# Kernel optimization log

Measured on AMD Instinct MI355X. Metric: run time of the kernel, lower is better.

The kernel has to match this reference:

```python
import jax, jax.numpy as jnp
import numpy as np
import math

# Static config (mirrors init_kwargs)
E, B, S, D, F, HMAX = 8, 4, 1024, 1024, 4096, 8
W = 768                      # active slimmable width (multiple giving integer head_dim)
H = max(1, W * HMAX // D)    # = 6 heads at width 768
HD = W // H                  # = 128
TOPK = 2
EPS = 1e-6


def setup_inputs() -> dict:
    key = jax.random.key(0)
    ks = jax.random.split(key, 14)
    sd = 1.0 / math.sqrt(D)
    sf = 1.0 / math.sqrt(F)
    return {
        "x":  jax.random.normal(ks[0], (B, S, D), jnp.float32),
        "wr": jax.random.normal(ks[1], (D, E), jnp.float32) * sd,
        "qw": jax.random.normal(ks[2], (E, D, D), jnp.float32) * sd,
        "qb": jax.random.normal(ks[3], (E, D), jnp.float32) * sd,
        "kw": jax.random.normal(ks[4], (E, D, D), jnp.float32) * sd,
        "kb": jax.random.normal(ks[5], (E, D), jnp.float32) * sd,
        "vw": jax.random.normal(ks[6], (E, D, D), jnp.float32) * sd,
        "vb": jax.random.normal(ks[7], (E, D), jnp.float32) * sd,
        "ow": jax.random.normal(ks[8], (E, D, D), jnp.float32) * sd,
        "ob": jax.random.normal(ks[9], (E, D), jnp.float32) * sd,
        "w1": jax.random.normal(ks[10], (E, F, D), jnp.float32) * sd,
        "b1": jax.random.normal(ks[11], (E, F), jnp.float32) * sd,
        "w2": jax.random.normal(ks[12], (E, D, F), jnp.float32) * sf,
        "b2": jax.random.normal(ks[13], (E, D), jnp.float32) * sf,
    }


def _slim_linear(x, w, b, in_w, out_w):
    # SlimmableLinear: dynamically slice max-size weight/bias to active widths
    return x @ w[:out_w, :in_w].T + b[:out_w]


def _rms_norm(x):
    # SlimmableExpert._layer_norm: RMS normalization (no mean-subtract, no affine)
    var = jnp.mean(jnp.square(x), axis=-1, keepdims=True)
    return x / jnp.sqrt(var + EPS)


def _expert_fwd(x_s, qw, qb, kw, kb, vw, vb, ow, ob, w1, b1, w2, b2):
    # x_s: [B, S, W]  (already sliced to active width)
    # --- slimmable self-attention at width W ---
    q = _slim_linear(x_s, qw, qb, W, W).reshape(B, S, H, HD).transpose(0, 2, 1, 3)
    k = _slim_linear(x_s, kw, kb, W, W).reshape(B, S, H, HD).transpose(0, 2, 1, 3)
    v = _slim_linear(x_s, vw, vb, W, W).reshape(B, S, H, HD).transpose(0, 2, 1, 3)
    scores = jnp.einsum('bhqd,bhkd->bhqk', q, k) / math.sqrt(HD)   # [B,H,S,S]
    attn = jax.nn.softmax(scores, axis=-1)
    ao = jnp.einsum('bhqk,bhkd->bhqd', attn, v)
    ao = ao.transpose(0, 2, 1, 3).reshape(B, S, W)
    ao = _slim_linear(ao, ow, ob, W, W)
    x1 = _rms_norm(x_s + ao)
    # --- slimmable FFN: W -> F (full) -> W, exact GELU (torch default) ---
    h = jax.nn.gelu(_slim_linear(x1, w1, b1, W, F), approximate=False)
    f = _slim_linear(h, w2, b2, F, W)
    return _rms_norm(x1 + f)   # [B,S,W]


def reference(x, wr, qw, qb, kw, kb, vw, vb, ow, ob, w1, b1, w2, b2):
    # Router: softmax over experts, top-k dispatch with renormalized gates
    logits = jnp.einsum('bsd,de->bse', x, wr)            # [B,S,E]
    probs = jax.nn.softmax(logits, axis=-1)
    topv, topi = jax.lax.top_k(probs, TOPK)              # [B,S,K]
    topv = topv / jnp.sum(topv, axis=-1, keepdims=True)
    bi = jnp.arange(B)[:, None, None]
    si = jnp.arange(S)[None, :, None]
    gate = jnp.zeros((B, S, E), x.dtype).at[bi, si, topi].set(topv)  # sparse gate

    # Slice tokens to active width (width embedding skipped: closest stored
    # width 736 != 768, per source shape-match check)
    x_s = x[..., :W]
    outs = []
    for e in range(E):   # small fixed expert count; bounds peak memory
        outs.append(_expert_fwd(x_s, qw[e], qb[e], kw[e], kb[e], vw[e], vb[e],
                                ow[e], ob[e], w1[e], b1[e], w2[e], b2[e]))
    eo = jnp.stack(outs, axis=0)                          # [E,B,S,W]
    out_w = jnp.einsum('bse,ebsw->bsw', gate, eo)         # gate-weighted combine
    # Zero-pad sliced width back to full model dim (per SlimmableExpert)
    out = jnp.concatenate(
        [out_w, jnp.zeros((B, S, D - W), x.dtype)], axis=-1)
    return out
```

## Files before the change

### kernel.cpp

```cpp
#include <hip/hip_runtime.h>
#include <cstdint>

#define NE 8
#define NB 4
#define NS 1024
#define ND 1024
#define NF 4096
#define NW 768
#define NH 6
#define NHD 128
#define NTOK 4096
#define NBH 24
#define RCAP 10496
#define VSTRIDE ((size_t)NTOK * NW)
#define EPS 1e-6f

typedef unsigned short ush;
typedef __attribute__((ext_vector_type(8))) short short8;
typedef __attribute__((ext_vector_type(4))) float f32x4;
typedef __attribute__((ext_vector_type(4))) unsigned short u16x4;

typedef const __attribute__((address_space(1))) void gvoid_t;
typedef __attribute__((address_space(3))) void lvoid_t;

__device__ __forceinline__ void gload16(const void* g, void* l) {
  __builtin_amdgcn_global_load_lds((gvoid_t*)g, (lvoid_t*)l, 16, 0, 0);
}

__device__ __forceinline__ ush f2b(float f) {
  union { float f; uint32_t u; } x; x.f = f;
  uint32_t r = x.u + 0x7fffu + ((x.u >> 16) & 1u);
  return (ush)(r >> 16);
}
__device__ __forceinline__ float b2f(ush u) {
  union { uint32_t u; float f; } x; x.u = (uint32_t)u << 16;
  return x.f;
}
__device__ __forceinline__ int prefix_sum(const int* __restrict__ c, int n) {
  int s = 0;
#pragma unroll 1
  for (int i = 0; i < n; ++i) s += c[i];
  return s;
}

__global__ __launch_bounds__(256, 4)
void router_kernel(const float* __restrict__ x, const float* __restrict__ wr,
                   float* __restrict__ gate, int* __restrict__ inv) {
  int lane = threadIdx.x & 63, wave = threadIdx.x >> 6;
  int t = blockIdx.x * 4 + wave;
  float acc[NE] = {};
  for (int i = 0; i < 16; ++i) {
    int d = lane + i * 64;
    float xv = x[(size_t)t * ND + d];
    const float* wp = wr + (size_t)d * NE;
    float4 w0 = *(const float4*)wp, w1 = *(const float4*)(wp + 4);
    acc[0] += xv * w0.x; acc[1] += xv * w0.y; acc[2] += xv * w0.z; acc[3] += xv * w0.w;
    acc[4] += xv * w1.x; acc[5] += xv * w1.y; acc[6] += xv * w1.z; acc[7] += xv * w1.w;
  }
#pragma unroll
  for (int e = 0; e < NE; ++e)
    for (int m = 1; m < 64; m <<= 1) acc[e] += __shfl_xor(acc[e], m);
  int i1 = 0; float v1 = acc[0];
#pragma unroll
  for (int e = 1; e < NE; ++e) if (acc[e] > v1) { v1 = acc[e]; i1 = e; }
  int i2 = -1; float v2 = -3.0e38f;
#pragma unroll
  for (int e = 0; e < NE; ++e) if (e != i1 && acc[e] > v2) { v2 = acc[e]; i2 = e; }
  float p2 = __expf(v2 - v1);
  float g1 = 1.0f / (1.0f + p2), g2 = p2 / (1.0f + p2);
  if (lane < NE)
    gate[(size_t)t * NE + lane] = (lane == i1) ? g1 : ((lane == i2) ? g2 : 0.0f);
  if (lane < 2) inv[t * 2 + lane] = -1;
}

__global__ __launch_bounds__(1024, 1)
void build_index(const float* __restrict__ gate, int* __restrict__ cnt64s,
                 int* __restrict__ idx_all, int* __restrict__ inv) {
  int e = blockIdx.x >> 2, b = blockIdx.x & 3;
  int s = threadIdx.x, t = b * 1024 + s;
  bool on = gate[(size_t)t * NE + e] > 0.0f;
  idx_all[(e * 4 + b) * 1024 + s] = (b * 1024) | (int)0x80000000;
  __shared__ int wsum[16], wbase[16];
  unsigned long long mask = __ballot(on);
  int lane = s & 63, wv = s >> 6;
  if (lane == 0) wsum[wv] = __popcll(mask);
  __syncthreads();
  if (s == 0) {
    int acc = 0;
    for (int i = 0; i < 16; ++i) { wbase[i] = acc; acc += wsum[i]; }
    cnt64s[e * 4 + b] = (acc + 63) & ~63;
  }
  __syncthreads();
  if (on) {
    int pos = wbase[wv] + __popcll(mask & ((1ull << lane) - 1ull));
    idx_all[(e * 4 + b) * 1024 + pos] = t;
    int k = 0;
#pragma unroll
    for (int j = 0; j < NE; ++j) k += (j < e && gate[(size_t)t * NE + j] > 0.0f);
    inv[t * 2 + k] = (e << 12) | pos;
  }
}

__global__ __launch_bounds__(256, 4)
void cast_all(const float* __restrict__ x,
              const float* __restrict__ qw, const float* __restrict__ kw,
              const float* __restrict__ vw, const float* __restrict__ ow,
              const float* __restrict__ w1, const float* __restrict__ w2,
              ush* __restrict__ xs,
              ush* __restrict__ dq, ush* __restrict__ dk, ush* __restrict__ dv,
              ush* __restrict__ dwo, ush* __restrict__ d1, ush* __restrict__ d2) {
  int y = blockIdx.y;
  if (y == 8) {
    const int n4 = NTOK * NW / 4;
    for (int u = blockIdx.x * 256 + threadIdx.x; u < n4; u += gridDim.x * 256) {
      int r = u / (NW / 4), c = u - r * (NW / 4);
      float4 v = *(const float4*)(x + (size_t)r * ND + c * 4);
      u16x4 o; o.x = f2b(v.x); o.y = f2b(v.y); o.z = f2b(v.z); o.w = f2b(v.w);
      *(u16x4*)(xs + (size_t)u * 4) = o;
    }
    return;
  }
  const int e = y;
  const int Q4 = 147456;
  const int W14 = 786432;
  const int total = 4 * Q4 + 2 * W14;
  const float* qe = qw + (size_t)e * ND * ND;
  const float* ke = kw + (size_t)e * ND * ND;
  const float* ve = vw + (size_t)e * ND * ND;
  const float* oe = ow + (size_t)e * ND * ND;
  const float* w1e = w1 + (size_t)e * NF * ND;
  const float* w2e = w2 + (size_t)e * ND * NF;
  ush* dqe = dq + (size_t)e * NW * NW;
  ush* dke = dk + (size_t)e * NW * NW;
  ush* dve = dv + (size_t)e * NW * NW;
  ush* doe = dwo + (size_t)e * NW * NW;
  ush* d1e = d1 + (size_t)e * NF * NW;
  ush* d2e = d2 + (size_t)e * NW * NF;
  for (int u = blockIdx.x * 256 + threadIdx.x; u < total; u += gridDim.x * 256) {
    const float* src; ush* dst; int ldsrc, cols4, rel;
    if (u < 4 * Q4) {
      int which = u / Q4; rel = u - which * Q4;
      src = (which == 0) ? qe : (which == 1) ? ke : (which == 2) ? ve : oe;
      dst = (which == 0) ? dqe : (which == 1) ? dke : (which == 2) ? dve : doe;
      ldsrc = 1024; cols4 = 192;
    } else if (u < 4 * Q4 + W14) {
      rel = u - 4 * Q4; src = w1e; dst = d1e; ldsrc = 1024; cols4 = 192;
    } else {
      rel = u - 4 * Q4 - W14; src = w2e; dst = d2e; ldsrc = 4096; cols4 = 1024;
    }
    int r = rel / cols4, c = rel - r * cols4;
    float4 v = *(const float4*)(src + (size_t)r * ldsrc + (size_t)c * 4);
    u16x4 o; o.x = f2b(v.x); o.y = f2b(v.y); o.z = f2b(v.z); o.w = f2b(v.w);
    *(u16x4*)(dst + (size_t)rel * 4) = o;
  }
}

#define BM 128
#define BN 128
#define BK 64

__device__ __forceinline__ float gelu_exact(float v) {
  return 0.5f * v * (1.0f + erff(v * 0.70710678118654752f));
}

__global__ __launch_bounds__(256, 3)
void qkv_gemm(const ush* __restrict__ A,
              const ush* __restrict__ wqb, const ush* __restrict__ wkb,
              const ush* __restrict__ wvb,
              const float* __restrict__ qbias, const float* __restrict__ kbias,
              const float* __restrict__ vbias,
              ush* __restrict__ qg, ush* __restrict__ kg, ush* __restrict__ vtg,
              const int* __restrict__ cnt64s, const int* __restrict__ idx_all) {
  const int bid = blockIdx.x;
  const int e = bid & 7, wi = bid >> 3;
  const int bn = wi % 6, bm = (wi / 6) % 32, w = wi / 192;
  int sb = 0, cnt = 0;
  if (w == 0) {
    int sec = e * 4 + (bm >> 3);
    cnt = cnt64s[sec];
    if (((bm & 7) * 128) >= cnt) return;
    sb = prefix_sum(cnt64s, sec);
  }
  const ush* Bw = ((w == 0) ? wqb : (w == 1) ? wkb : wvb) + (size_t)e * NW * NW;
  const float* bias = ((w == 0) ? qbias : (w == 1) ? kbias : vbias) + (size_t)e * ND;

  __shared__ __align__(16) ush As[BM * BK];
  __shared__ __align__(16) ush Bs[BN * BK];

  const int tid = threadIdx.x, lane = tid & 63, wave = tid >> 6;
  const int lr = lane & 15, lg = lane >> 4;
  const int wr = wave >> 1, wc = wave & 1;

  int rowIdx[4];
#pragma unroll
  for (int p = 0; p < 4; ++p) {
    if (w == 0) {
      int lrow = (bm & 7) * 128 + p * 32 + (tid >> 3);
      rowIdx[p] = idx_all[(e * 4 + (bm >> 3)) * 1024 + lrow] & 0x7fffffff;
    } else {
      rowIdx[p] = bm * BM + p * 32 + (tid >> 3);
    }
  }

  f32x4 acc[4][4] = {};
  for (int kt = 0; kt < NW / BK; ++kt) {
    __syncthreads();
#pragma unroll
    for (int p = 0; p < 4; ++p) {
      int o = p * 4096 + tid * 16;
      int row = o >> 7, cb = o & 127;
      int cbs = cb ^ ((row & 7) << 4);
      gload16((const char*)A + ((size_t)rowIdx[p] * NW + (size_t)kt * BK) * 2 + cbs,
              (char*)As + o);
      gload16((const char*)Bw + ((size_t)(bn * BN + row) * NW + (size_t)kt * BK) * 2 + cbs,
              (char*)Bs + o);
    }
    __syncthreads();
#pragma unroll
    for (int kk = 0; kk < 2; ++kk) {
      short8 af[4], bfr[4];
#pragma unroll
      for (int i = 0; i < 4; ++i) {
        int rowa = wr * 64 + i * 16 + lr;
        af[i] = *(const short8*)((const char*)As + rowa * 128 +
                                 (((kk * 64 + lg * 16)) ^ ((rowa & 7) << 4)));
        int rowb = wc * 64 + i * 16 + lr;
        bfr[i] = *(const short8*)((const char*)Bs + rowb * 128 +
                                  (((kk * 64 + lg * 16)) ^ ((rowb & 7) << 4)));
      }
#pragma unroll
      for (int i = 0; i < 4; ++i)
#pragma unroll
        for (int j = 0; j < 4; ++j)
          acc[i][j] = __builtin_amdgcn_mfma_f32_16x16x32_bf16(af[i], bfr[j], acc[i][j], 0, 0, 0);
    }
  }

#pragma unroll
  for (int i = 0; i < 4; ++i) {
    int lm16 = (bm & 7) * 128 + wr * 64 + i * 16;
    int m0 = bm * BM + wr * 64 + i * 16 + lg * 4;
#pragma unroll
    for (int j = 0; j < 4; ++j) {
      int n = bn * BN + wc * 64 + j * 16 + lr;
      float bb = bias[n];
      if (w == 0) {
        if (lm16 < cnt) {
          int grow = sb + lm16 + lg * 4;
#pragma unroll
          for (int r = 0; r < 4; ++r)
            qg[(size_t)(grow + r) * NW + n] = f2b(acc[i][j][r] + bb);
        }
      } else if (w == 1) {
        ush* o = kg + (size_t)e * NTOK * NW;
#pragma unroll
        for (int r = 0; r < 4; ++r)
          o[(size_t)(m0 + r) * NW + n] = f2b(acc[i][j][r] + bb);
      } else {
        int b_ = m0 >> 10, s0 = m0 & 1023, h_ = n >> 7, d = n & 127;
        u16x4 wv_;
#pragma unroll
        for (int r = 0; r < 4; ++r) wv_[r] = f2b(acc[i][j][r] + bb);
        *(u16x4*)(vtg + (size_t)e * VSTRIDE +
                  ((size_t)(b_ * NH + h_) * NHD + d) * NS + s0) = wv_;
      }
    }
  }
}

__global__ __launch_bounds__(256, 3)
void attn2(const ush* __restrict__ Qg, const ush* __restrict__ Kg,
           const ush* __restrict__ VTg,
           ush* __restrict__ po, float* __restrict__ mlm, float* __restrict__ mll,
           const int* __restrict__ cnt64s) {
  const int bid = blockIdx.x;
  const int e = bid & 7, wi = bid >> 3;
  const int qb = wi & 15, yy = wi >> 4;
  const int bh = yy >> 2, half = yy & 3;
  const int b = bh / NH, h = bh % NH;
  const int sec = e * 4 + b;
  const int cnt = cnt64s[sec];
  if (qb * 64 >= cnt) return;
  const int sb = prefix_sum(cnt64s, sec);

  __shared__ __align__(16) ush Ks[64 * 128];
  __shared__ __align__(16) ush VTs[128 * 64];
  __shared__ __align__(16) ush Ps[4 * 16 * 64];

  const int tid = threadIdx.x, lane = tid & 63, wave = tid >> 6;
  const int lr = lane & 15, lg = lane >> 4;
  const int k0 = half * 256;
  const float cexp = 1.4426950408889634f / sqrtf((float)NHD);

  const ush* Ke = Kg + (size_t)e * NTOK * NW;
  const ush* Ve = VTg + (size_t)e * VSTRIDE;

  int growq = sb + qb * 64 + wave * 16 + lr;
  short8 qf[4];
#pragma unroll
  for (int kk = 0; kk < 4; ++kk)
    qf[kk] = *(const short8*)(Qg + (size_t)growq * NW + h * NHD + kk * 32 + lg * 8);

  f32x4 accv[8] = {};
  float mr[4] = {-3.0e38f, -3.0e38f, -3.0e38f, -3.0e38f};
  float ls[4] = {};

  for (int kt = 0; kt < 4; ++kt) {
    __syncthreads();
#pragma unroll
    for (int p = 0; p < 4; ++p) {
      int o = p * 4096 + tid * 16;
      int row = o >> 8, cb = o & 255;
      gload16((const char*)Ke + ((size_t)(b * NS + k0 + kt * 64 + row) * NW + h * NHD) * 2 +
                  (cb ^ ((row & 7) << 4)),
              (char*)Ks + o);
    }
#pragma unroll
    for (int p = 0; p < 4; ++p) {
      int o = p * 4096 + tid * 16;
      int d = o >> 7, cb = o & 127;
      gload16((const char*)Ve + ((size_t)((b * NH + h) * NHD + d) * NS + k0 + kt * 64) * 2 +
                  (cb ^ ((d & 7) << 4)),
              (char*)VTs + o);
    }
    __syncthreads();

    f32x4 s[4] = {};
#pragma unroll
    for (int kg2 = 0; kg2 < 4; ++kg2)
#pragma unroll
      for (int kk = 0; kk < 4; ++kk) {
        int row = kg2 * 16 + lr;
        short8 kf = *(const short8*)((const char*)Ks + row * 256 +
                                     ((kk * 64 + lg * 16) ^ ((row & 7) << 4)));
        s[kg2] = __builtin_amdgcn_mfma_f32_16x16x32_bf16(qf[kk], kf, s[kg2], 0, 0, 0);
      }

    float mt[4];
#pragma unroll
    for (int r = 0; r < 4; ++r) {
      float m0 = fmaxf(fmaxf(s[0][r], s[1][r]), fmaxf(s[2][r], s[3][r]));
#pragma unroll
      for (int mm = 1; mm < 16; mm <<= 1) m0 = fmaxf(m0, __shfl_xor(m0, mm));
      mt[r] = m0;
    }
    bool need = (mt[0] > mr[0] + 8.f) || (mt[1] > mr[1] + 8.f) ||
                (mt[2] > mr[2] + 8.f) || (mt[3] > mr[3] + 8.f);
    if (__any(need)) {
#pragma unroll
      for (int r = 0; r < 4; ++r) {
        float mn = fmaxf(mr[r], mt[r]);
        float sc = exp2f((mr[r] - mn) * cexp);
        mr[r] = mn; ls[r] *= sc;
#pragma unroll
        for (int dg = 0; dg < 8; ++dg) accv[dg][r] *= sc;
      }
    }

    char* pw = (char*)Ps + wave * 2048;
#pragma unroll
    for (int kg2 = 0; kg2 < 4; ++kg2)
#pragma unroll
      for (int r = 0; r < 4; ++r) {
        float p = exp2f((s[kg2][r] - mr[r]) * cexp);
        ls[r] += p;
        int row = lg * 4 + r;
        *(ush*)(pw + row * 128 + (((kg2 * 16 + lr) * 2) ^ ((row & 7) << 4))) = f2b(p);
      }
    short8 pf[2];
#pragma unroll
    for (int kk2 = 0; kk2 < 2; ++kk2)
      pf[kk2] = *(const short8*)(pw + lr * 128 + ((kk2 * 64 + lg * 16) ^ ((lr & 7) << 4)));

#pragma unroll
    for (int dg = 0; dg < 8; ++dg) {
      int d = dg * 16 + lr;
#pragma unroll
      for (int kk2 = 0; kk2 < 2; ++kk2) {
        short8 vf = *(const short8*)((const char*)VTs + d * 128 +
                                     ((kk2 * 64 + lg * 16) ^ ((d & 7) << 4)));
        accv[dg] = __builtin_amdgcn_mfma_f32_16x16x32_bf16(pf[kk2], vf, accv[dg], 0, 0, 0);
      }
    }
  }

#pragma unroll
  for (int r = 0; r < 4; ++r)
#pragma unroll
    for (int mm = 1; mm < 16; mm <<= 1) ls[r] += __shfl_xor(ls[r], mm);

#pragma unroll
  for (int r = 0; r < 4; ++r) {
    int growr = sb + qb * 64 + wave * 16 + lg * 4 + r;
#pragma unroll
    for (int dg = 0; dg < 8; ++dg)
      po[((size_t)(growr * NH + h) * 4 + half) * NHD + dg * 16 + lr] = f2b(accv[dg][r]);
  }
  if (lr == 0) {
#pragma unroll
    for (int r = 0; r < 4; ++r) {
      int growr = sb + qb * 64 + wave * 16 + lg * 4 + r;
      mlm[(size_t)(growr * NH + h) * 4 + half] = mr[r];
      mll[(size_t)(growr * NH + h) * 4 + half] = ls[r];
    }
  }
}

__global__ __launch_bounds__(256, 4)
void attn_combine(const ush* __restrict__ po, const float* __restrict__ mlm,
                  const float* __restrict__ mll, ush* __restrict__ ao,
                  const int* __restrict__ cnt64s) {
  const float cexp = 1.4426950408889634f / sqrtf((float)NHD);
  int Rtot = prefix_sum(cnt64s, 32);
  int idx = blockIdx.x * 256 + threadIdx.x;
  int row = idx >> 4, dq = idx & 15;
  int grow = row / NH, h = row - grow * NH;
  if (grow >= Rtot) return;
  float m[4], l[4], M = -3.0e38f;
#pragma unroll
  for (int hh = 0; hh < 4; ++hh) {
    m[hh] = mlm[(size_t)row * 4 + hh];
    l[hh] = mll[(size_t)row * 4 + hh];
    M = fmaxf(M, m[hh]);
  }
  float L = 0.0f, w[4];
#pragma unroll
  for (int hh = 0; hh < 4; ++hh) { w[hh] = exp2f((m[hh] - M) * cexp); L += l[hh] * w[hh]; }
  float inv_ = 1.0f / L;
  float o[8] = {};
#pragma unroll
  for (int hh = 0; hh < 4; ++hh) {
    short8 v = *(const short8*)(po + ((size_t)row * 4 + hh) * NHD + dq * 8);
#pragma unroll
    for (int j = 0; j < 8; ++j) o[j] += b2f((ush)v[j]) * w[hh];
  }
  short8 res;
#pragma unroll
  for (int j = 0; j < 8; ++j) res[j] = (short)f2b(o[j] * inv_);
  *(short8*)(ao + (size_t)grow * NW + h * NHD + dq * 8) = res;
}

template <int EPI>
__global__ __launch_bounds__(256, 3)
void csr_gemm(const ush* __restrict__ A, const ush* __restrict__ Ball,
              const float* __restrict__ biasAll, ush* __restrict__ out,
              int N, int Kld, int klen, int nbn, int nbm, int nsplit,
              int strideBe, int biasStride,
              const int* __restrict__ cnt64s) {
  const int bid = blockIdx.x;
  const int e = bid & 7, wi = bid >> 3;
  const int bn = wi % nbn, bm = (wi / nbn) % nbm, s = wi / (nbn * nbm);
  const int Re = cnt64s[e * 4] + cnt64s[e * 4 + 1] + cnt64s[e * 4 + 2] + cnt64s[e * 4 + 3];
  if (bm * BM >= Re) return;
  const int ebase = prefix_sum(cnt64s, e * 4);
  const ush* Bw = Ball + (size_t)e * strideBe;
  const float* bias = (s == 0) ? biasAll + (size_t)e * biasStride : nullptr;
  const int koff = s * klen;
  ush* outp = out + (size_t)s * RCAP * N;

  __shared__ __align__(16) ush As[BM * BK];
  __shared__ __align__(16) ush Bs[BN * BK];

  const int tid = threadIdx.x, lane = tid & 63, wave = tid >> 6;
  const int lr = lane & 15, lg = lane >> 4;
  const int wr = wave >> 1, wc = wave & 1;

  f32x4 acc[4][4] = {};
  const int nkt = klen / BK;
  for (int kt = 0; kt < nkt; ++kt) {
    __syncthreads();
#pragma unroll
    for (int p = 0; p < 4; ++p) {
      int o = p * 4096 + tid * 16;
      int row = o >> 7, cb = o & 127;
      int cbs = cb ^ ((row & 7) << 4);
      gload16((const char*)A + ((size_t)(ebase + bm * BM + row) * Kld + koff + (size_t)kt * BK) * 2 + cbs,
              (char*)As + o);
      gload16((const char*)Bw + ((size_t)(bn * BN + row) * Kld + koff + (size_t)kt * BK) * 2 + cbs,
              (char*)Bs + o);
    }
    __syncthreads();
#pragma unroll
    for (int kk = 0; kk < 2; ++kk) {
      short8 af[4], bfr[4];
#pragma unroll
      for (int i = 0; i < 4; ++i) {
        int rowa = wr * 64 + i * 16 + lr;
        af[i] = *(const short8*)((const char*)As + rowa * 128 +
                                 (((kk * 64 + lg * 16)) ^ ((rowa & 7) << 4)));
        int rowb = wc * 64 + i * 16 + lr;
        bfr[i] = *(const short8*)((const char*)Bs + rowb * 128 +
                                  (((kk * 64 + lg * 16)) ^ ((rowb & 7) << 4)));
      }
#pragma unroll
      for (int i = 0; i < 4; ++i)
#pragma unroll
        for (int j = 0; j < 4; ++j)
          acc[i][j] = __builtin_amdgcn_mfma_f32_16x16x32_bf16(af[i], bfr[j], acc[i][j], 0, 0, 0);
    }
  }

#pragma unroll
  for (int i = 0; i < 4; ++i) {
    int lm16 = bm * BM + wr * 64 + i * 16;
    if (lm16 >= Re) continue;
#pragma unroll
    for (int j = 0; j < 4; ++j) {
      int n = bn * BN + wc * 64 + j * 16 + lr;
      float bb = bias ? bias[n] : 0.0f;
      int row0 = ebase + lm16 + lg * 4;
#pragma unroll
      for (int r = 0; r < 4; ++r) {
        float v = acc[i][j][r] + bb;
        if (EPI == 2) v = gelu_exact(v);
        outp[(size_t)(row0 + r) * N + n] = f2b(v);
      }
    }
  }
}

__global__ __launch_bounds__(256, 4)
void rmsnorm_res(const float* __restrict__ x, const ush* __restrict__ ooP,
                 ush* __restrict__ x1b, const int* __restrict__ cnt64s,
                 const int* __restrict__ idx_all) {
  int r = blockIdx.x;
  int base = 0, sec = -1, loc = 0;
#pragma unroll 1
  for (int i = 0; i < 32; ++i) {
    int cc = cnt64s[i];
    if (sec < 0 && r < base + cc) { sec = i; loc = r - base; }
    base += cc;
  }
  if (sec < 0) return;
  int t = idx_all[sec * 1024 + loc] & 0x7fffffff;
  __shared__ float red[4];
  int c = threadIdx.x, lane = c & 63, wave = c >> 6;
  float v[3]; float ss = 0.0f;
#pragma unroll
  for (int i = 0; i < 3; ++i) {
    int col = c + i * 256;
    float a = x[(size_t)t * ND + col] + b2f(ooP[(size_t)r * NW + col]) +
              b2f(ooP[(size_t)RCAP * NW + (size_t)r * NW + col]);
    v[i] = a; ss += a * a;
  }
#pragma unroll
  for (int m = 1; m < 64; m <<= 1) ss += __shfl_xor(ss, m);
  if (lane == 0) red[wave] = ss;
  __syncthreads();
  float tot = red[0] + red[1] + red[2] + red[3];
  float scale = rsqrtf(tot / (float)NW + EPS);
#pragma unroll
  for (int i = 0; i < 3; ++i) {
    int col = c + i * 256;
    x1b[(size_t)r * NW + col] = f2b(v[i] * scale);
  }
}

__global__ __launch_bounds__(256, 4)
void final_token(const ush* __restrict__ x1b, const ush* __restrict__ ffp,
                 const float* __restrict__ gate, const int* __restrict__ inv,
                 const int* __restrict__ cnt64s, float* __restrict__ out) {
  int t = blockIdx.x, c = threadIdx.x, lane = c & 63, wave = c >> 6;
  __shared__ float red[4];
  float acc[3] = {0.0f, 0.0f, 0.0f};
#pragma unroll 1
  for (int k = 0; k < 2; ++k) {
    int v = inv[t * 2 + k];
    if (v >= 0) {
      int e = v >> 12, pos = v & 0xfff;
      int b = t >> 10;
      int grow = prefix_sum(cnt64s, e * 4 + b) + pos;
      float g = gate[(size_t)t * NE + e];
      float vv[3]; float ss = 0.0f;
#pragma unroll
      for (int i = 0; i < 3; ++i) {
        int col = c + i * 256;
        float f = b2f(ffp[(size_t)grow * NW + col]) +
                  b2f(ffp[(size_t)RCAP * NW + (size_t)grow * NW + col]) +
                  b2f(ffp[2 * (size_t)RCAP * NW + (size_t)grow * NW + col]) +
                  b2f(ffp[3 * (size_t)RCAP * NW + (size_t)grow * NW + col]);
        float a = b2f(x1b[(size_t)grow * NW + col]) + f;
        vv[i] = a; ss += a * a;
      }
#pragma unroll
      for (int m = 1; m < 64; m <<= 1) ss += __shfl_xor(ss, m);
      if (lane == 0) red[wave] = ss;
      __syncthreads();
      float tot = red[0] + red[1] + red[2] + red[3];
      float scale = rsqrtf(tot / (float)NW + EPS) * g;
#pragma unroll
      for (int i = 0; i < 3; ++i) acc[i] += vv[i] * scale;
      __syncthreads();
    }
  }
#pragma unroll
  for (int i = 0; i < 3; ++i) out[(size_t)t * ND + c + i * 256] = acc[i];
  out[(size_t)t * ND + 768 + c] = 0.0f;
}

extern "C" void kernel_launch(void* const* d_in, const int* in_sizes, int n_in,
                              void* d_out, int out_size, void* d_ws, size_t ws_size,
                              hipStream_t stream) {
  (void)in_sizes; (void)n_in; (void)ws_size; (void)out_size;
  const float* x  = (const float*)d_in[0];
  const float* wr = (const float*)d_in[1];
  const float* qw = (const float*)d_in[2];
  const float* qbias = (const float*)d_in[3];
  const float* kw = (const float*)d_in[4];
  const float* kbias = (const float*)d_in[5];
  const float* vw = (const float*)d_in[6];
  const float* vbias = (const float*)d_in[7];
  const float* ow = (const float*)d_in[8];
  const float* obias = (const float*)d_in[9];
  const float* w1 = (const float*)d_in[10];
  const float* b1 = (const float*)d_in[11];
  const float* w2 = (const float*)d_in[12];
  const float* b2 = (const float*)d_in[13];
  float* out = (float*)d_out;
  char* ws = (char*)d_ws;

  size_t off = 0;
  auto alloc = [&](size_t bytes) {
    void* p = ws + off;
    off += (bytes + 255) & ~(size_t)255;
    return p;
  };
  float* gate = (float*)alloc((size_t)NTOK * NE * 4);
  int* cnt64s = (int*)alloc(32 * 4);
  int* idx_all = (int*)alloc((size_t)NE * NTOK * 4);
  int* inv = (int*)alloc((size_t)NTOK * 2 * 4);
  ush* xs  = (ush*)alloc((size_t)NTOK * NW * 2);
  ush* wqb = (ush*)alloc((size_t)NE * NW * NW * 2);
  ush* wkb = (ush*)alloc((size_t)NE * NW * NW * 2);
  ush* wvb = (ush*)alloc((size_t)NE * NW * NW * 2);
  ush* wob = (ush*)alloc((size_t)NE * NW * NW * 2);
  ush* w1b = (ush*)alloc((size_t)NE * NF * NW * 2);
  ush* w2b = (ush*)alloc((size_t)NE * NW * NF * 2);
  ush* x1b = (ush*)alloc((size_t)RCAP * NW * 2);
  char* arena1 = (char*)alloc((size_t)RCAP * NF * 2);
  ush* qg  = (ush*)arena1;
  ush* po  = (ush*)(arena1 + 16121856);
  float* mlm = (float*)(arena1 + 80609280);
  float* mll = (float*)(arena1 + 81616896);
  ush* hb  = (ush*)arena1;
  char* arena2 = (char*)alloc(112852992);
  ush* kg  = (ush*)arena2;
  ush* vtg = (ush*)(arena2 + 50331648);
  ush* aog = (ush*)arena2;
  ush* ooP = (ush*)(arena2 + 16121856);
  ush* ffp = (ush*)(arena2 + 48365568);

  router_kernel<<<dim3(NTOK / 4), 256, 0, stream>>>(x, wr, gate, inv);
  build_index<<<dim3(NE * NB), 1024, 0, stream>>>(gate, cnt64s, idx_all, inv);
  cast_all<<<dim3(288, 9), 256, 0, stream>>>(x, qw, kw, vw, ow, w1, w2,
                                             xs, wqb, wkb, wvb, wob, w1b, w2b);

  qkv_gemm<<<dim3(8 * 576), 256, 0, stream>>>(
      xs, wqb, wkb, wvb, qbias, kbias, vbias, qg, kg, vtg, cnt64s, idx_all);

  attn2<<<dim3(8 * 1536), 256, 0, stream>>>(qg, kg, vtg, po, mlm, mll, cnt64s);
  attn_combine<<<dim3(RCAP * NH * 16 / 256), 256, 0, stream>>>(po, mlm, mll, aog, cnt64s);

  csr_gemm<0><<<dim3(8 * 384), 256, 0, stream>>>(
      aog, wob, obias, ooP, NW, NW, 384, 6, 32, 2, NW * NW, ND, cnt64s);

  rmsnorm_res<<<dim3(RCAP), 256, 0, stream>>>(x, ooP, x1b, cnt64s, idx_all);

  csr_gemm<2><<<dim3(8 * 1024), 256, 0, stream>>>(
      x1b, w1b, b1, hb, NF, NW, NW, 32, 32, 1, NF * NW, NF, cnt64s);

  csr_gemm<0><<<dim3(8 * 768), 256, 0, stream>>>(
      hb, w2b, b2, ffp, NW, NF, 1024, 6, 32, 4, NW * NF, ND, cnt64s);

  final_token<<<dim3(NTOK), 256, 0, stream>>>(x1b, ffp, gate, inv, cnt64s, out);
}
```

Before: 609.3 us.

## Double-buffer LDS tiles in qkv and csr GEMMs to overlap loads with MFMA

Both the QKV GEMM and the CSR expert GEMM now use two LDS buffers per operand. The next K tile is issued with direct global-to-LDS loads while MFMAs run on the current tile, and there is one barrier per iteration instead of two. Launch bounds drop from 3 to 2 blocks per CU because LDS use doubles to 64KB per block. The csr_gemm block index mapping is also reordered so consecutive blocks walk M before N, which changes weight tile reuse in cache.

```diff
diff --git a/kernel.cpp b/kernel.cpp
--- a/kernel.cpp
+++ b/kernel.cpp
@@ -163,7 +163,7 @@
   return 0.5f * v * (1.0f + erff(v * 0.70710678118654752f));
 }
 
-__global__ __launch_bounds__(256, 3)
+__global__ __launch_bounds__(256, 2)
 void qkv_gemm(const ush* __restrict__ A,
               const ush* __restrict__ wqb, const ush* __restrict__ wkb,
               const ush* __restrict__ wvb,
@@ -184,8 +184,8 @@
   const ush* Bw = ((w == 0) ? wqb : (w == 1) ? wkb : wvb) + (size_t)e * NW * NW;
   const float* bias = ((w == 0) ? qbias : (w == 1) ? kbias : vbias) + (size_t)e * ND;
 
-  __shared__ __align__(16) ush As[BM * BK];
-  __shared__ __align__(16) ush Bs[BN * BK];
+  __shared__ __align__(16) ush As[2][BM * BK];
+  __shared__ __align__(16) ush Bs[2][BN * BK];
 
   const int tid = threadIdx.x, lane = tid & 63, wave = tid >> 6;
   const int lr = lane & 15, lg = lane >> 4;
@@ -202,30 +202,36 @@
     }
   }
 
-  f32x4 acc[4][4] = {};
-  for (int kt = 0; kt < NW / BK; ++kt) {
-    __syncthreads();
+  auto stage = [&](int buf, int kt) {
 #pragma unroll
     for (int p = 0; p < 4; ++p) {
       int o = p * 4096 + tid * 16;
       int row = o >> 7, cb = o & 127;
       int cbs = cb ^ ((row & 7) << 4);
       gload16((const char*)A + ((size_t)rowIdx[p] * NW + (size_t)kt * BK) * 2 + cbs,
-              (char*)As + o);
+              (char*)As[buf] + o);
       gload16((const char*)Bw + ((size_t)(bn * BN + row) * NW + (size_t)kt * BK) * 2 + cbs,
-              (char*)Bs + o);
-    }
-    __syncthreads();
+              (char*)Bs[buf] + o);
+    }
+  };
+
+  f32x4 acc[4][4] = {};
+  const int nkt = NW / BK;
+  stage(0, 0);
+  __syncthreads();
+  for (int kt = 0; kt < nkt; ++kt) {
+    const int cur = kt & 1;
+    if (kt + 1 < nkt) stage(cur ^ 1, kt + 1);
 #pragma unroll
     for (int kk = 0; kk < 2; ++kk) {
       short8 af[4], bfr[4];
 #pragma unroll
       for (int i = 0; i < 4; ++i) {
         int rowa = wr * 64 + i * 16 + lr;
-        af[i] = *(const short8*)((const char*)As + rowa * 128 +
+        af[i] = *(const short8*)((const char*)As[cur] + rowa * 128 +
                                  (((kk * 64 + lg * 16)) ^ ((rowa & 7) << 4)));
         int rowb = wc * 64 + i * 16 + lr;
-        bfr[i] = *(const short8*)((const char*)Bs + rowb * 128 +
+        bfr[i] = *(const short8*)((const char*)Bs[cur] + rowb * 128 +
                                   (((kk * 64 + lg * 16)) ^ ((rowb & 7) << 4)));
       }
 #pragma unroll
@@ -234,6 +240,7 @@
         for (int j = 0; j < 4; ++j)
           acc[i][j] = __builtin_amdgcn_mfma_f32_16x16x32_bf16(af[i], bfr[j], acc[i][j], 0, 0, 0);
     }
+    __syncthreads();
   }
 
 #pragma unroll
@@ -441,7 +448,7 @@
 }
 
 template <int EPI>
-__global__ __launch_bounds__(256, 3)
+__global__ __launch_bounds__(256, 2)
 void csr_gemm(const ush* __restrict__ A, const ush* __restrict__ Ball,
               const float* __restrict__ biasAll, ush* __restrict__ out,
               int N, int Kld, int klen, int nbn, int nbm, int nsplit,
@@ -449,7 +456,7 @@
               const int* __restrict__ cnt64s) {
   const int bid = blockIdx.x;
   const int e = bid & 7, wi = bid >> 3;
-  const int bn = wi % nbn, bm = (wi / nbn) % nbm, s = wi / (nbn * nbm);
+  const int bm = wi % nbm, bn = (wi / nbm) % nbn, s = wi / (nbm * nbn);
   const int Re = cnt64s[e * 4] + cnt64s[e * 4 + 1] + cnt64s[e * 4 + 2] + cnt64s[e * 4 + 3];
   if (bm * BM >= Re) return;
   const int ebase = prefix_sum(cnt64s, e * 4);
@@ -458,38 +465,43 @@
   const int koff = s * klen;
   ush* outp = out + (size_t)s * RCAP * N;
 
-  __shared__ __align__(16) ush As[BM * BK];
-  __shared__ __align__(16) ush Bs[BN * BK];
+  __shared__ __align__(16) ush As[2][BM * BK];
+  __shared__ __align__(16) ush Bs[2][BN * BK];
 
   const int tid = threadIdx.x, lane = tid & 63, wave = tid >> 6;
   const int lr = lane & 15, lg = lane >> 4;
   const int wr = wave >> 1, wc = wave & 1;
 
-  f32x4 acc[4][4] = {};
-  const int nkt = klen / BK;
-  for (int kt = 0; kt < nkt; ++kt) {
-    __syncthreads();
+  auto stage = [&](int buf, int kt) {
 #pragma unroll
     for (int p = 0; p < 4; ++p) {
       int o = p * 4096 + tid * 16;
       int row = o >> 7, cb = o & 127;
       int cbs = cb ^ ((row & 7) << 4);
       gload16((const char*)A + ((size_t)(ebase + bm * BM + row) * Kld + koff + (size_t)kt * BK) * 2 + cbs,
-              (char*)As + o);
+              (char*)As[buf] + o);
       gload16((const char*)Bw + ((size_t)(bn * BN + row) * Kld + koff + (size_t)kt * BK) * 2 + cbs,
-              (char*)Bs + o);
-    }
-    __syncthreads();
+              (char*)Bs[buf] + o);
+    }
+  };
+
+  f32x4 acc[4][4] = {};
+  const int nkt = klen / BK;
+  stage(0, 0);
+  __syncthreads();
+  for (int kt = 0; kt < nkt; ++kt) {
+    const int cur = kt & 1;
+    if (kt + 1 < nkt) stage(cur ^ 1, kt + 1);
 #pragma unroll
     for (int kk = 0; kk < 2; ++kk) {
       short8 af[4], bfr[4];
 #pragma unroll
       for (int i = 0; i < 4; ++i) {
         int rowa = wr * 64 + i * 16 + lr;
-        af[i] = *(const short8*)((const char*)As + rowa * 128 +
+        af[i] = *(const short8*)((const char*)As[cur] + rowa * 128 +
                                  (((kk * 64 + lg * 16)) ^ ((rowa & 7) << 4)));
         int rowb = wc * 64 + i * 16 + lr;
-        bfr[i] = *(const short8*)((const char*)Bs + rowb * 128 +
+        bfr[i] = *(const short8*)((const char*)Bs[cur] + rowb * 128 +
                                   (((kk * 64 + lg * 16)) ^ ((rowb & 7) << 4)));
       }
 #pragma unroll
@@ -498,6 +510,7 @@
         for (int j = 0; j < 4; ++j)
           acc[i][j] = __builtin_amdgcn_mfma_f32_16x16x32_bf16(af[i], bfr[j], acc[i][j], 0, 0, 0);
     }
+    __syncthreads();
   }
 
 #pragma unroll
```

Result: slower. 791.6 us (+29.9%).

## Triple-buffer LDS staging with async global loads in qkv and csr GEMMs

Applied to the files above, without the earlier changes.

Replaces the single-buffered BK=64 load/compute loop in the QKV and CSR GEMM kernels with a three-slot LDS ring of K=32 tiles, prefetching two tiles ahead using global_load_lds. Manual s_waitcnt vmcnt and s_barrier replace the double __syncthreads, so loads overlap MFMA work. A new staging geometry remaps rows and the XOR swizzle for the narrower K tile. LDS per block grows to 48KB, which may limit occupancy at 3 blocks per CU.

```diff
diff --git a/kernel.cpp b/kernel.cpp
--- a/kernel.cpp
+++ b/kernel.cpp
@@ -42,6 +42,7 @@
   for (int i = 0; i < n; ++i) s += c[i];
   return s;
 }
+
 
 __global__ __launch_bounds__(256, 4)
 void router_kernel(const float* __restrict__ x, const float* __restrict__ wr,
@@ -157,10 +158,16 @@
 
 #define BM 128
 #define BN 128
-#define BK 64
 
 __device__ __forceinline__ float gelu_exact(float v) {
   return 0.5f * v * (1.0f + erff(v * 0.70710678118654752f));
+}
+
+__device__ __forceinline__ void stage_geom(int tid, int c, int& row, int& kb) {
+  int v = (c & 1) * 32 + (tid >> 3);
+  int b67 = ((tid >> 2) & 1) ^ ((v >> 2) & 1);
+  row = v + 64 * b67;
+  kb = ((tid ^ v) & 3) << 4;
 }
 
 __global__ __launch_bounds__(256, 3)
@@ -184,56 +191,74 @@
   const ush* Bw = ((w == 0) ? wqb : (w == 1) ? wkb : wvb) + (size_t)e * NW * NW;
   const float* bias = ((w == 0) ? qbias : (w == 1) ? kbias : vbias) + (size_t)e * ND;
 
-  __shared__ __align__(16) ush As[BM * BK];
-  __shared__ __align__(16) ush Bs[BN * BK];
+  __shared__ __align__(16) char LDS[3 * 16384];
 
   const int tid = threadIdx.x, lane = tid & 63, wave = tid >> 6;
   const int lr = lane & 15, lg = lane >> 4;
   const int wr = wave >> 1, wc = wave & 1;
 
-  int rowIdx[4];
-#pragma unroll
-  for (int p = 0; p < 4; ++p) {
-    if (w == 0) {
-      int lrow = (bm & 7) * 128 + p * 32 + (tid >> 3);
-      rowIdx[p] = idx_all[(e * 4 + (bm >> 3)) * 1024 + lrow] & 0x7fffffff;
+  size_t srcOff[4];
+#pragma unroll
+  for (int c = 0; c < 4; ++c) {
+    int row, kb; stage_geom(tid, c, row, kb);
+    int gRow;
+    if (c < 2) {
+      if (w == 0) {
+        int lrow = (bm & 7) * 128 + row;
+        gRow = idx_all[(e * 4 + (bm >> 3)) * 1024 + lrow] & 0x7fffffff;
+      } else {
+        gRow = bm * BM + row;
+      }
     } else {
-      rowIdx[p] = bm * BM + p * 32 + (tid >> 3);
-    }
-  }
+      gRow = bn * BN + row;
+    }
+    srcOff[c] = (size_t)gRow * (NW * 2) + kb;
+  }
+
+  int offA[4], offB[4];
+#pragma unroll
+  for (int i = 0; i < 4; ++i) {
+    offA[i] = (i * 16 + lr) * 128 + (((wr << 6) | (lg << 4)) ^ ((lr & 7) << 4));
+    offB[i] = (i * 16 + lr) * 128 + (((wc << 6) | (lg << 4)) ^ ((lr & 7) << 4)) + 8192;
+  }
+
+  auto stg = [&](int slot, int kt) {
+    size_t kOff = (size_t)kt * 64;
+    char* dst = LDS + slot * 16384;
+#pragma unroll
+    for (int c = 0; c < 4; ++c) {
+      const char* src = (c < 2) ? (const char*)A + srcOff[c] + kOff
+                                : (const char*)Bw + srcOff[c] + kOff;
+      gload16(src, dst + c * 4096 + tid * 16);
+    }
+  };
 
   f32x4 acc[4][4] = {};
-  for (int kt = 0; kt < NW / BK; ++kt) {
-    __syncthreads();
-#pragma unroll
-    for (int p = 0; p < 4; ++p) {
-      int o = p * 4096 + tid * 16;
-      int row = o >> 7, cb = o & 127;
-      int cbs = cb ^ ((row & 7) << 4);
-      gload16((const char*)A + ((size_t)rowIdx[p] * NW + (size_t)kt * BK) * 2 + cbs,
-              (char*)As + o);
-      gload16((const char*)Bw + ((size_t)(bn * BN + row) * NW + (size_t)kt * BK) * 2 + cbs,
-              (char*)Bs + o);
-    }
-    __syncthreads();
-#pragma unroll
-    for (int kk = 0; kk < 2; ++kk) {
-      short8 af[4], bfr[4];
-#pragma unroll
-      for (int i = 0; i < 4; ++i) {
-        int rowa = wr * 64 + i * 16 + lr;
-        af[i] = *(const short8*)((const char*)As + rowa * 128 +
-                                 (((kk * 64 + lg * 16)) ^ ((rowa & 7) << 4)));
-        int rowb = wc * 64 + i * 16 + lr;
-        bfr[i] = *(const short8*)((const char*)Bs + rowb * 128 +
-                                  (((kk * 64 + lg * 16)) ^ ((rowb & 7) << 4)));
-      }
-#pragma unroll
-      for (int i = 0; i < 4; ++i)
-#pragma unroll
-        for (int j = 0; j < 4; ++j)
-          acc[i][j] = __builtin_amdgcn_mfma_f32_16x16x32_bf16(af[i], bfr[j], acc[i][j], 0, 0, 0);
-    }
+  const int nkt = NW / 32;
+  stg(0, 0); stg(1, 1);
+  asm volatile("s_waitcnt vmcnt(4)" ::: "memory");
+  asm volatile("s_barrier" ::: "memory");
+  int slot = 0;
+  for (int kt = 0; kt < nkt; ++kt) {
+    int s2 = slot + 2; if (s2 >= 3) s2 -= 3;
+    bool more = (kt + 2 < nkt);
+    if (more) stg(s2, kt + 2);
+    const char* base = LDS + slot * 16384;
+    short8 af[4], bfr[4];
+#pragma unroll
+    for (int i = 0; i < 4; ++i) {
+      af[i] = *(const short8*)(base + offA[i]);
+      bfr[i] = *(const short8*)(base + offB[i]);
+    }
+#pragma unroll
+    for (int i = 0; i < 4; ++i)
+#pragma unroll
+      for (int j = 0; j < 4; ++j)
+        acc[i][j] = __builtin_amdgcn_mfma_f32_16x16x32_bf16(af[i], bfr[j], acc[i][j], 0, 0, 0);
+    if (more) asm volatile("s_waitcnt vmcnt(4)" ::: "memory");
+    else      asm volatile("s_waitcnt vmcnt(0)" ::: "memory");
+    asm volatile("s_barrier" ::: "memory");
+    slot = (slot == 2) ? 0 : slot + 1;
   }
 
 #pragma unroll
@@ -458,46 +483,64 @@
   const int koff = s * klen;
   ush* outp = out + (size_t)s * RCAP * N;
 
-  __shared__ __align__(16) ush As[BM * BK];
-  __shared__ __align__(16) ush Bs[BN * BK];
+  __shared__ __align__(16) char LDS[3 * 16384];
 
   const int tid = threadIdx.x, lane = tid & 63, wave = tid >> 6;
   const int lr = lane & 15, lg = lane >> 4;
   const int wr = wave >> 1, wc = wave & 1;
 
+  size_t srcOff[4];
+#pragma unroll
+  for (int c = 0; c < 4; ++c) {
+    int row, kb; stage_geom(tid, c, row, kb);
+    int gRow = (c < 2) ? (ebase + bm * BM + row) : (bn * BN + row);
+    srcOff[c] = (size_t)gRow * (Kld * 2) + (size_t)koff * 2 + kb;
+  }
+
+  int offA[4], offB[4];
+#pragma unroll
+  for (int i = 0; i < 4; ++i) {
+    offA[i] = (i * 16 + lr) * 128 + (((wr << 6) | (lg << 4)) ^ ((lr & 7) << 4));
+    offB[i] = (i * 16 + lr) * 128 + (((wc << 6) | (lg << 4)) ^ ((lr & 7) << 4)) + 8192;
+  }
+
+  auto stg = [&](int slot, int kt) {
+    size_t kOff = (size_t)kt * 64;
+    char* dst = LDS + slot * 16384;
+#pragma unroll
+    for (int c = 0; c < 4; ++c) {
+      const char* src = (c < 2) ? (const char*)A + srcOff[c] + kOff
+                                : (const char*)Bw + srcOff[c] + kOff;
+      gload16(src, dst + c * 4096 + tid * 16);
+    }
+  };
+
   f32x4 acc[4][4] = {};
-  const int nkt = klen / BK;
+  const int nkt = klen / 32;
+  stg(0, 0); stg(1, 1);
+  asm volatile("s_waitcnt vmcnt(4)" ::: "memory");
+  asm volatile("s_barrier" ::: "memory");
+  int slot = 0;
   for (int kt = 0; kt < nkt; ++kt) {
-    __syncthreads();
-#pragma unroll
-    for (int p = 0; p < 4; ++p) {
-      int o = p * 4096 + tid * 16;
-      int row = o >> 7, cb = o & 127;
-      int cbs = cb ^ ((row & 7) << 4);
-      gload16((const char*)A + ((size_t)(ebase + bm * BM + row) * Kld + koff + (size_t)kt * BK) * 2 + cbs,
-              (char*)As + o);
-      gload16((const char*)Bw + ((size_t)(bn * BN + row) * Kld + koff + (size_t)kt * BK) * 2 + cbs,
-              (char*)Bs + o);
-    }
-    __syncthreads();
-#pragma unroll
-    for (int kk = 0; kk < 2; ++kk) {
-      short8 af[4], bfr[4];
-#pragma unroll
-      for (int i = 0; i < 4; ++i) {
-        int rowa = wr * 64 + i * 16 + lr;
-        af[i] = *(const short8*)((const char*)As + rowa * 128 +
-                                 (((kk * 64 + lg * 16)) ^ ((rowa & 7) << 4)));
-        int rowb = wc * 64 + i * 16 + lr;
-        bfr[i] = *(const short8*)((const char*)Bs + rowb * 128 +
-                                  (((kk * 64 + lg * 16)) ^ ((rowb & 7) << 4)));
-      }
-#pragma unroll
-      for (int i = 0; i < 4; ++i)
-#pragma unroll
-        for (int j = 0; j < 4; ++j)
-          acc[i][j] = __builtin_amdgcn_mfma_f32_16x16x32_bf16(af[i], bfr[j], acc[i][j], 0, 0, 0);
-    }
+    int s2 = slot + 2; if (s2 >= 3) s2 -= 3;
+    bool more = (kt + 2 < nkt);
+    if (more) stg(s2, kt + 2);
+    const char* base = LDS + slot * 16384;
+    short8 af[4], bfr[4];
+#pragma unroll
+    for (int i = 0; i < 4; ++i) {
+      af[i] = *(const short8*)(base + offA[i]);
+      bfr[i] = *(const short8*)(base + offB[i]);
+    }
+#pragma unroll
+    for (int i = 0; i < 4; ++i)
+#pragma unroll
+      for (int j = 0; j < 4; ++j)
+        acc[i][j] = __builtin_amdgcn_mfma_f32_16x16x32_bf16(af[i], bfr[j], acc[i][j], 0, 0, 0);
+    if (more) asm volatile("s_waitcnt vmcnt(4)" ::: "memory");
+    else      asm volatile("s_waitcnt vmcnt(0)" ::: "memory");
+    asm volatile("s_barrier" ::: "memory");
+    slot = (slot == 2) ? 0 : slot + 1;
   }
 
 #pragma unroll
```

New measurement: 617.8 us. No clear change (+1.4%).
